# Performance work log

Measured on AMD Instinct MI355X. Metric: run time of the kernel, lower is better.

Reference implementation:

```python
import jax, jax.numpy as jnp
import numpy as np

NUM_EMBEDDINGS = 8192
EMBEDDING_DIM = 256
COMMITMENT_COST = 0.25


def setup_inputs() -> dict:
    key = jax.random.key(0)
    k1, k2 = jax.random.split(key)
    inputs = jax.random.normal(k1, (32, 32, 32, EMBEDDING_DIM), dtype=jnp.float32)
    # flax nn.initializers.uniform(scale=1/num_embeddings) -> U[0, scale)
    embeddings = jax.random.uniform(
        k2, (NUM_EMBEDDINGS, EMBEDDING_DIM), dtype=jnp.float32,
        minval=0.0, maxval=1.0 / NUM_EMBEDDINGS)
    return {"inputs": inputs, "embeddings": embeddings}


def reference(inputs, embeddings):
    flat_input = inputs.reshape(-1, EMBEDDING_DIM)  # [N, D]
    distances = (jnp.sum(flat_input ** 2, axis=1, keepdims=True)
                 - 2.0 * jnp.dot(flat_input, embeddings.T)
                 + jnp.sum(embeddings ** 2, axis=1)[None, :])
    encoding_indices = jnp.argmin(distances, axis=1)  # [N]
    quantized = embeddings[encoding_indices]  # [N, D]

    e_latent_loss = jnp.mean((jax.lax.stop_gradient(quantized) - flat_input) ** 2)
    q_latent_loss = jnp.mean((quantized - jax.lax.stop_gradient(flat_input)) ** 2)
    vq_loss = q_latent_loss + COMMITMENT_COST * e_latent_loss

    # straight-through estimator
    quantized_st = flat_input + jax.lax.stop_gradient(quantized - flat_input)
    quantized_st = quantized_st.reshape(inputs.shape)

    # perplexity via codebook usage histogram (avoids materializing one-hot)
    counts = jnp.zeros((NUM_EMBEDDINGS,), dtype=flat_input.dtype).at[encoding_indices].add(1.0)
    avg_probs = counts / flat_input.shape[0]
    perplexity = jnp.exp(-jnp.sum(avg_probs * jnp.log(avg_probs + 1e-10)))

    return quantized_st, vq_loss, perplexity, encoding_indices
```

## Files before the change

### kernel.cpp

```cpp
#include <hip/hip_runtime.h>
#include <math.h>

#pragma clang fp contract(off)

#define N_ROWS 32768
#define DIM    256
#define K_EMB  8192
#define BCAP   2048
#define NSUB   256

typedef float  f32x4  __attribute__((ext_vector_type(4)));
typedef short  bf16x8 __attribute__((ext_vector_type(8)));

__device__ __forceinline__ void gl_lds16(const uint4* g, uint4* l) {
  __builtin_amdgcn_global_load_lds(
      (const __attribute__((address_space(1))) unsigned int*)g,
      (__attribute__((address_space(3))) unsigned int*)l,
      16, 0, 0);
}

__device__ __forceinline__ unsigned bf_rne(float f) {
  unsigned u = __float_as_uint(f);
  return (u + 0x7fffu + ((u >> 16) & 1u)) >> 16;
}
__device__ __forceinline__ unsigned pack2(float lo, float hi) {
  return bf_rne(lo) | (bf_rne(hi) << 16);
}

__device__ __forceinline__ float np_pw128_sumsq(const float* __restrict__ a) {
  float4 v0 = *(const float4*)(a);
  float4 v1 = *(const float4*)(a + 4);
  float r0 = v0.x*v0.x, r1 = v0.y*v0.y, r2 = v0.z*v0.z, r3 = v0.w*v0.w;
  float r4 = v1.x*v1.x, r5 = v1.y*v1.y, r6 = v1.z*v1.z, r7 = v1.w*v1.w;
  for (int i = 8; i < 128; i += 8) {
    float4 w0 = *(const float4*)(a + i);
    float4 w1 = *(const float4*)(a + i + 4);
    r0 += w0.x*w0.x; r1 += w0.y*w0.y; r2 += w0.z*w0.z; r3 += w0.w*w0.w;
    r4 += w1.x*w1.x; r5 += w1.y*w1.y; r6 += w1.z*w1.z; r7 += w1.w*w1.w;
  }
  return ((r0+r1)+(r2+r3))+((r4+r5)+(r6+r7));
}

__global__ __launch_bounds__(256) void vq_sumsq(const float* __restrict__ src,
                                                float* __restrict__ dst, int nrows) {
  int gid  = blockIdx.x * 256 + threadIdx.x;
  int row  = gid >> 1, half = gid & 1;
  if (row >= nrows) return;
  float s = np_pw128_sumsq(src + (size_t)row * DIM + half * 128);
  float o = __shfl_xor(s, 1);
  if (half == 0) dst[row] = s + o;
}

__global__ __launch_bounds__(256) void vq_prep(
    const float* __restrict__ X, const float* __restrict__ E,
    float* __restrict__ A, float* __restrict__ C, uint4* __restrict__ Eb,
    unsigned* __restrict__ hist, unsigned* __restrict__ bcnt,
    unsigned* __restrict__ ovf, unsigned long long* __restrict__ best) {
  const int b = blockIdx.x;
  if (b < 1024) {
    int t = b * 256 + threadIdx.x;
    int tile = t >> 6, l = t & 63;
    int cfg = tile >> 3, ks = tile & 7;
    int code = cfg * 16 + (l & 15);
    int k0 = (ks * 4 + (l >> 4)) * 8;
    const float4* src = (const float4*)(E + (size_t)code * DIM + k0);
    float4 a = src[0], bb = src[1];
    uint4 o;
    o.x = pack2(a.x, a.y);  o.y = pack2(a.z, a.w);
    o.z = pack2(bb.x, bb.y); o.w = pack2(bb.z, bb.w);
    Eb[t] = o;
  } else if (b < 1280) {
    int gid = (b - 1024) * 256 + threadIdx.x;
    int row = gid >> 1, half = gid & 1;
    float s = np_pw128_sumsq(X + (size_t)row * DIM + half * 128);
    float o = __shfl_xor(s, 1);
    if (half == 0) A[row] = s + o;
  } else if (b < 1344) {
    int gid = (b - 1280) * 256 + threadIdx.x;
    int row = gid >> 1, half = gid & 1;
    float s = np_pw128_sumsq(E + (size_t)row * DIM + half * 128);
    float o = __shfl_xor(s, 1);
    if (half == 0) C[row] = s + o;
  } else {
    int i = (b - 1344) * 256 + threadIdx.x;
    ovf[i]  = 0u;
    best[i] = ~0ull;
    if (i < K_EMB) hist[i] = 0u;
    if (i < NSUB)  bcnt[i] = 0u;
  }
}

__global__ __launch_bounds__(256)
__attribute__((amdgpu_waves_per_eu(2, 2)))
void vq_mfma_slice(
    const float* __restrict__ X, const uint4* __restrict__ Eb,
    unsigned short* __restrict__ submax_t) {
  __shared__ __align__(16) unsigned short es[2][64 * 256];

  const int tid   = threadIdx.x;
  const int lane  = tid & 63, w = tid >> 6;
  const int lr    = lane & 15, lg = lane >> 4;
  const int wcg   = w & 1;
  const int wxg   = w >> 1;
  const int rb    = blockIdx.x >> 1;
  const int slice = blockIdx.x & 1;
  const int row0  = rb * 128;

  const uint4* ebase = Eb + (size_t)slice * 131072;

#pragma unroll
  for (int i = 0; i < 8; ++i) {
    int u = tid + i * 256;
    gl_lds16(ebase + u, ((uint4*)&es[0][0]) + u);
  }

  bf16x8 bx[4][8];
#pragma unroll
  for (int rf = 0; rf < 4; ++rf) {
    const float* xr = X + (size_t)(row0 + wxg * 64 + rf * 16 + lr) * DIM;
#pragma unroll
    for (int ks = 0; ks < 8; ++ks) {
      int k0 = (ks * 4 + lg) * 8;
      float4 a = *(const float4*)(xr + k0);
      float4 b = *(const float4*)(xr + k0 + 4);
      uint4 o;
      o.x = pack2(a.x, a.y); o.y = pack2(a.z, a.w);
      o.z = pack2(b.x, b.y); o.w = pack2(b.z, b.w);
      bx[rf][ks] = *(bf16x8*)&o;
    }
  }
  __syncthreads();

  for (int c = 0; c < 64; ++c) {
    const int cur = c & 1;
    if (c + 1 < 64) {
#pragma unroll
      for (int i = 0; i < 8; ++i) {
        int u = tid + i * 256;
        gl_lds16(ebase + (size_t)(c + 1) * 2048 + u, ((uint4*)&es[cur ^ 1][0]) + u);
      }
    }

    f32x4 acc[2][4];
#pragma unroll
    for (int ce = 0; ce < 2; ++ce)
#pragma unroll
      for (int rf = 0; rf < 4; ++rf)
        acc[ce][rf] = (f32x4){0.f, 0.f, 0.f, 0.f};

    const unsigned short* eb = &es[cur][0];
#pragma unroll
    for (int ks = 0; ks < 8; ++ks) {
      bf16x8 ev0 = *(const bf16x8*)(eb + (((wcg * 2 + 0) * 8 + ks) * 64 + lane) * 8);
      bf16x8 ev1 = *(const bf16x8*)(eb + (((wcg * 2 + 1) * 8 + ks) * 64 + lane) * 8);
#pragma unroll
      for (int rf = 0; rf < 4; ++rf) {
        acc[0][rf] = __builtin_amdgcn_mfma_f32_16x16x32_bf16(ev0, bx[rf][ks], acc[0][rf], 0, 0, 0);
        acc[1][rf] = __builtin_amdgcn_mfma_f32_16x16x32_bf16(ev1, bx[rf][ks], acc[1][rf], 0, 0, 0);
      }
    }

    const int sub = slice * 128 + c * 2 + wcg;
#pragma unroll
    for (int rf = 0; rf < 4; ++rf) {
      float m = acc[0][rf][0];
#pragma unroll
      for (int ce = 0; ce < 2; ++ce)
#pragma unroll
        for (int rg = 0; rg < 4; ++rg)
          if (ce | rg) m = fmaxf(m, acc[ce][rf][rg]);
      m = fmaxf(m, __shfl_xor(m, 16));
      m = fmaxf(m, __shfl_xor(m, 32));
      if (lg == 0) {
        int qi = (int)((m + 0.0625f) * 524288.0f);
        qi = qi < 0 ? 0 : (qi > 65535 ? 65535 : qi);
        submax_t[(size_t)sub * N_ROWS + row0 + wxg * 64 + rf * 16 + lr] =
            (unsigned short)qi;
      }
    }

    asm volatile("s_waitcnt vmcnt(4)" ::: "memory");
    __builtin_amdgcn_s_barrier();
  }
}

__global__ __launch_bounds__(256) void vq_flag(
    const unsigned short* __restrict__ submax_t, const float* __restrict__ A,
    unsigned* __restrict__ bcnt, unsigned short* __restrict__ buckets,
    unsigned* __restrict__ ovf) {
  __shared__ unsigned cntA[NSUB], baseS[NSUB], cntC[NSUB];
  const int t   = threadIdx.x;
  const int row = blockIdx.x * 256 + t;
  cntA[t] = 0u; cntC[t] = 0u;
  __syncthreads();

  int mq = 0;
  for (int s = 0; s < NSUB; ++s) {
    int q = submax_t[(size_t)s * N_ROWS + row];
    mq = q > mq ? q : mq;
  }
  const int wq   = (int)((sqrtf(A[row]) * 4e-6f + 9.6e-5f) * 524288.0f) + 2;
  const int thrq = mq - wq;

  for (int s = 0; s < NSUB; ++s)
    if ((int)submax_t[(size_t)s * N_ROWS + row] >= thrq) atomicAdd(&cntA[s], 1u);
  __syncthreads();

  baseS[t] = atomicAdd(&bcnt[t], cntA[t]);
  __syncthreads();

  for (int s = 0; s < NSUB; ++s) {
    if ((int)submax_t[(size_t)s * N_ROWS + row] >= thrq) {
      unsigned p = baseS[s] + atomicAdd(&cntC[s], 1u);
      if (p < BCAP) buckets[s * BCAP + p] = (unsigned short)row;
      else          ovf[row] = 1u;
    }
  }
}

__global__ __launch_bounds__(256) void vq_exact(
    const float* __restrict__ X, const float* __restrict__ E,
    const float* __restrict__ A, const float* __restrict__ C,
    const unsigned* __restrict__ bcnt, const unsigned short* __restrict__ buckets,
    unsigned long long* __restrict__ best) {
  __shared__ float e_lds[32][260];
  __shared__ float xr[4][4][256];
  const int tid  = threadIdx.x;
  const int lane = tid & 63, w = tid >> 6;
  const int bk   = blockIdx.x >> 2, q4 = blockIdx.x & 3;

#pragma unroll
  for (int i = 0; i < 8; ++i) {
    int u = tid + i * 256;
    int code = u >> 6, koff = (u & 63) * 4;
    float4 v = *(const float4*)(E + (size_t)(bk * 32 + code) * DIM + koff);
    *(float4*)(&e_lds[code][koff]) = v;
  }
  __syncthreads();

  int n = (int)bcnt[bk]; if (n > BCAP) n = BCAP;
  const int   half = lane >> 5, c32 = lane & 31;
  const int   j  = bk * 32 + c32;
  const float cj = C[j];

  for (int p0 = q4 * 16 + w * 4; p0 < n; p0 += 64) {
    int valid[4], rows[4];
#pragma unroll
    for (int k = 0; k < 4; ++k) {
      int pk = p0 + k;
      valid[k] = (pk < n);
      rows[k]  = buckets[(size_t)bk * BCAP + (pk < n ? pk : p0)];
    }
#pragma unroll
    for (int k = 0; k < 4; ++k)
      *(float4*)(&xr[w][k][lane * 4]) =
          *(const float4*)(X + (size_t)rows[k] * DIM + lane * 4);
    asm volatile("s_waitcnt lgkmcnt(0)" ::: "memory");

    float acc0 = 0.f, acc1 = 0.f;
    const float* xa = &xr[w][half][0];
    const float* xb = &xr[w][half + 2][0];
#pragma unroll 4
    for (int kq = 0; kq < 64; ++kq) {
      float4 ev = *(const float4*)(&e_lds[c32][kq * 4]);
      float4 x0 = *(const float4*)(xa + kq * 4);
      float4 x1 = *(const float4*)(xb + kq * 4);
      acc0 = fmaf(x0.x, ev.x, acc0); acc0 = fmaf(x0.y, ev.y, acc0);
      acc0 = fmaf(x0.z, ev.z, acc0); acc0 = fmaf(x0.w, ev.w, acc0);
      acc1 = fmaf(x1.x, ev.x, acc1); acc1 = fmaf(x1.y, ev.y, acc1);
      acc1 = fmaf(x1.z, ev.z, acc1); acc1 = fmaf(x1.w, ev.w, acc1);
    }
    float d0 = (A[rows[half]]     - 2.0f * acc0) + cj;
    float d1 = (A[rows[half + 2]] - 2.0f * acc1) + cj;
    int   j0 = j, j1 = j;
#pragma unroll
    for (int mm = 1; mm < 32; mm <<= 1) {
      float od = __shfl_xor(d0, mm); int oj = __shfl_xor(j0, mm);
      if (od < d0 || (od == d0 && oj < j0)) { d0 = od; j0 = oj; }
      od = __shfl_xor(d1, mm); oj = __shfl_xor(j1, mm);
      if (od < d1 || (od == d1 && oj < j1)) { d1 = od; j1 = oj; }
    }
    if (c32 == 0) {
      if (valid[half])
        atomicMin(&best[rows[half]],
                  ((unsigned long long)__float_as_uint(d0) << 32) | (unsigned)j0);
      if (valid[half + 2])
        atomicMin(&best[rows[half + 2]],
                  ((unsigned long long)__float_as_uint(d1) << 32) | (unsigned)j1);
    }
  }
}

__global__ __launch_bounds__(256) void vq_finish(
    const float* __restrict__ X, const float* __restrict__ E,
    const float* __restrict__ A, const float* __restrict__ C,
    const unsigned* __restrict__ ovf, const unsigned long long* __restrict__ best,
    int* __restrict__ idx_out, float* __restrict__ idxf_out) {
  int row  = blockIdx.x * 256 + threadIdx.x;
  int lane = threadIdx.x & 63;
  unsigned o = ovf[row];
  if (!o) {
    int j = (int)(best[row] & 0xffffffffu);
    idx_out[row]  = j;
    idxf_out[row] = (float)j;
  }
  unsigned long long m = __ballot(o != 0u);
  while (m) {
    int src  = __ffsll((long long)m) - 1;
    int orow = __shfl(row, src);
    const float a_r = A[orow];
    const float4* X4 = (const float4*)(X + (size_t)orow * DIM);
    float bd = INFINITY; int bj = 0x7fffffff;
    for (int jj = lane; jj < K_EMB; jj += 64) {
      const float4* E4 = (const float4*)(E + (size_t)jj * DIM);
      float acc = 0.f;
      for (int kb = 0; kb < 64; ++kb) {
        float4 xv = X4[kb], ev = E4[kb];
        acc = fmaf(xv.x, ev.x, acc); acc = fmaf(xv.y, ev.y, acc);
        acc = fmaf(xv.z, ev.z, acc); acc = fmaf(xv.w, ev.w, acc);
      }
      float d = (a_r - 2.0f * acc) + C[jj];
      if (d < bd || (d == bd && jj < bj)) { bd = d; bj = jj; }
    }
    for (int mm = 1; mm < 64; mm <<= 1) {
      float od = __shfl_xor(bd, mm);
      int   oj = __shfl_xor(bj, mm);
      if (od < bd || (od == bd && oj < bj)) { bd = od; bj = oj; }
    }
    if (lane == 0) { idx_out[orow] = bj; idxf_out[orow] = (float)bj; }
    m &= m - 1;
  }
}

__global__ __launch_bounds__(256) void vq_argmin(const float* __restrict__ X,
                                                 const float* __restrict__ E,
                                                 const float* __restrict__ A,
                                                 const float* __restrict__ C,
                                                 int* __restrict__ idx_out,
                                                 float* __restrict__ idxf_out) {
  __shared__ float4 xs4[64 * 64];
  const int tid  = threadIdx.x;
  const int rl   = tid >> 2;
  const int cg   = tid & 3;
  const int row0 = blockIdx.x * 64;

  const float4* Xg = (const float4*)(X + (size_t)row0 * DIM);
  for (int it = 0; it < 16; ++it) {
    int f4 = tid + it * 256;
    float4 v = Xg[f4];
    int r = f4 >> 6, kb = f4 & 63;
    xs4[r * 64 + (kb ^ (r & 7))] = v;
  }
  __syncthreads();

  const float a_r = A[row0 + rl];
  const int   swq = rl & 7;
  const float4* xrow = xs4 + rl * 64;

  float bd = INFINITY;
  int   bj = 0x7fffffff;

  for (int tile = 0; tile < K_EMB; tile += 16) {
    const int j0 = tile + cg * 4;
    const float4* e0 = (const float4*)(E + (size_t)(j0 + 0) * DIM);
    const float4* e1 = (const float4*)(E + (size_t)(j0 + 1) * DIM);
    const float4* e2 = (const float4*)(E + (size_t)(j0 + 2) * DIM);
    const float4* e3 = (const float4*)(E + (size_t)(j0 + 3) * DIM);
    float acc0 = 0.f, acc1 = 0.f, acc2 = 0.f, acc3 = 0.f;
#pragma unroll 4
    for (int kb = 0; kb < 64; ++kb) {
      const float4 xv = xrow[kb ^ swq];
      const float4 q0 = e0[kb], q1 = e1[kb], q2 = e2[kb], q3 = e3[kb];
      acc0 = fmaf(xv.x, q0.x, acc0); acc0 = fmaf(xv.y, q0.y, acc0);
      acc0 = fmaf(xv.z, q0.z, acc0); acc0 = fmaf(xv.w, q0.w, acc0);
      acc1 = fmaf(xv.x, q1.x, acc1); acc1 = fmaf(xv.y, q1.y, acc1);
      acc1 = fmaf(xv.z, q1.z, acc1); acc1 = fmaf(xv.w, q1.w, acc1);
      acc2 = fmaf(xv.x, q2.x, acc2); acc2 = fmaf(xv.y, q2.y, acc2);
      acc2 = fmaf(xv.z, q2.z, acc2); acc2 = fmaf(xv.w, q2.w, acc2);
      acc3 = fmaf(xv.x, q3.x, acc3); acc3 = fmaf(xv.y, q3.y, acc3);
      acc3 = fmaf(xv.z, q3.z, acc3); acc3 = fmaf(xv.w, q3.w, acc3);
    }
    const float d0 = (a_r - 2.0f * acc0) + C[j0 + 0];
    const float d1 = (a_r - 2.0f * acc1) + C[j0 + 1];
    const float d2 = (a_r - 2.0f * acc2) + C[j0 + 2];
    const float d3 = (a_r - 2.0f * acc3) + C[j0 + 3];
    if (d0 < bd) { bd = d0; bj = j0 + 0; }
    if (d1 < bd) { bd = d1; bj = j0 + 1; }
    if (d2 < bd) { bd = d2; bj = j0 + 2; }
    if (d3 < bd) { bd = d3; bj = j0 + 3; }
  }
  for (int m = 1; m < 4; m <<= 1) {
    float od = __shfl_xor(bd, m);
    int   oj = __shfl_xor(bj, m);
    if (od < bd || (od == bd && oj < bj)) { bd = od; bj = oj; }
  }
  if (cg == 0) {
    int row = row0 + rl;
    idx_out[row]  = bj;
    idxf_out[row] = (float)bj;
  }
}

__global__ __launch_bounds__(256) void vq_quant(const float* __restrict__ X,
                                                const float* __restrict__ E,
                                                const int* __restrict__ idx,
                                                float* __restrict__ out_qst,
                                                double* __restrict__ partials,
                                                unsigned* __restrict__ hist) {
  int gid  = blockIdx.x * 256 + threadIdx.x;
  int base = gid * 4;
  int row  = base >> 8;
  int k    = base & 255;
  int j    = idx[row];
  if (k == 0) atomicAdd(&hist[j], 1u);
  const float4 xv = *(const float4*)(X + (size_t)base);
  const float4 ev = *(const float4*)(E + (size_t)j * DIM + k);
  float4 o;
  float d0 = ev.x - xv.x, d1 = ev.y - xv.y, d2 = ev.z - xv.z, d3 = ev.w - xv.w;
  o.x = xv.x + d0; o.y = xv.y + d1; o.z = xv.z + d2; o.w = xv.w + d3;
  double s = (double)d0 * d0 + (double)d1 * d1 + (double)d2 * d2 + (double)d3 * d3;
  *(float4*)(out_qst + (size_t)base) = o;

  for (int m = 32; m; m >>= 1) s += __shfl_xor(s, m);
  __shared__ double wsum[4];
  int lane = threadIdx.x & 63, w = threadIdx.x >> 6;
  if (lane == 0) wsum[w] = s;
  __syncthreads();
  if (threadIdx.x == 0)
    partials[blockIdx.x] = (wsum[0] + wsum[1]) + (wsum[2] + wsum[3]);
}

__global__ void vq_zero(unsigned* counts) {
  int i = blockIdx.x * 256 + threadIdx.x;
  if (i < K_EMB) counts[i] = 0u;
}

__global__ __launch_bounds__(256) void vq_scalars(const double* __restrict__ partials,
                                                  const unsigned* __restrict__ counts,
                                                  float* __restrict__ out_loss,
                                                  float* __restrict__ out_perp) {
  __shared__ double red[256];
  int t = threadIdx.x;
  double s = 0.0;
  for (int i = t; i < 8192; i += 256) s += partials[i];
  red[t] = s;
  __syncthreads();
  for (int o = 128; o; o >>= 1) { if (t < o) red[t] += red[t + o]; __syncthreads(); }
  double mse = red[0] / (double)((size_t)N_ROWS * DIM);
  __syncthreads();

  double p = 0.0;
  for (int i = t; i < K_EMB; i += 256) {
    double pr = (double)counts[i] / (double)N_ROWS;
    p += pr * log(pr + 1e-10);
  }
  red[t] = p;
  __syncthreads();
  for (int o = 128; o; o >>= 1) { if (t < o) red[t] += red[t + o]; __syncthreads(); }
  if (t == 0) {
    float m = (float)mse;
    out_loss[0] = m + 0.25f * m;
    out_perp[0] = (float)exp(-red[0]);
  }
}

extern "C" void kernel_launch(void* const* d_in, const int* in_sizes, int n_in,
                              void* d_out, int out_size, void* d_ws, size_t ws_size,
                              hipStream_t stream) {
  const float* X = (const float*)d_in[0];
  const float* E = (const float*)d_in[1];
  float* out  = (float*)d_out;
  float* qst  = out;
  float* loss = out + 8388608;
  float* perp = out + 8388609;
  float* idxf = out + 8388610;

  float*    A        = (float*)d_ws;
  float*    C        = (float*)((char*)d_ws + 131072);
  int*      idx      = (int*)((char*)d_ws + 163840);
  unsigned* hist     = (unsigned*)((char*)d_ws + 294912);
  double*   partials = (double*)((char*)d_ws + 327680);

  if (ws_size >= 22807552) {
    unsigned long long* best = (unsigned long long*)((char*)d_ws + 393216);
    unsigned* ovf          = (unsigned*)((char*)d_ws + 655360);
    unsigned* bcnt         = (unsigned*)((char*)d_ws + 786432);
    unsigned short* bucket = (unsigned short*)((char*)d_ws + 787456);
    uint4*    Eb           = (uint4*)((char*)d_ws + 1836032);
    unsigned short* sm     = (unsigned short*)((char*)d_ws + 6030336);

    vq_prep       <<<1472, 256, 0, stream>>>(X, E, A, C, Eb, hist, bcnt, ovf, best);
    vq_mfma_slice <<<512,  256, 0, stream>>>(X, Eb, sm);
    vq_flag       <<<128,  256, 0, stream>>>(sm, A, bcnt, bucket, ovf);
    vq_exact      <<<1024, 256, 0, stream>>>(X, E, A, C, bcnt, bucket, best);
    vq_finish     <<<128,  256, 0, stream>>>(X, E, A, C, ovf, best, idx, idxf);
  } else {
    vq_zero   <<<32,  256, 0, stream>>>(hist);
    vq_sumsq  <<<256, 256, 0, stream>>>(X, A, N_ROWS);
    vq_sumsq  <<<64,  256, 0, stream>>>(E, C, K_EMB);
    vq_argmin <<<512, 256, 0, stream>>>(X, E, A, C, idx, idxf);
  }

  vq_quant  <<<8192, 256, 0, stream>>>(X, E, idx, qst, partials, hist);
  vq_scalars<<<1,    256, 0, stream>>>(partials, hist, loss, perp);
}
```

Before: 345.2 us.

## Fuse candidate flagging into MFMA slice kernel via last-block completion counter

Removes the separate vq_flag launch. Each row block's two slice CTAs bump a per-row-block counter, and the second one to finish scans the submax values for its 128 rows and writes the candidate buckets. The candidate window constant is also narrowed, which should shrink the bucket lists and the exact-rescoring work in vq_exact. The risks are a serialized tail in the MFMA kernel with only half the threads doing the flag work, and a tighter window that may miss true argmins.

```diff
diff --git a/kernel.cpp b/kernel.cpp
--- a/kernel.cpp
+++ b/kernel.cpp
@@ -25,6 +25,10 @@
 }
 __device__ __forceinline__ unsigned pack2(float lo, float hi) {
   return bf_rne(lo) | (bf_rne(hi) << 16);
+}
+
+__device__ __forceinline__ int window_q(float a) {
+  return (int)((sqrtf(a) * 4e-6f + 5.0e-5f) * 524288.0f) + 2;
 }
 
 __device__ __forceinline__ float np_pw128_sumsq(const float* __restrict__ a) {
@@ -55,7 +59,8 @@
     const float* __restrict__ X, const float* __restrict__ E,
     float* __restrict__ A, float* __restrict__ C, uint4* __restrict__ Eb,
     unsigned* __restrict__ hist, unsigned* __restrict__ bcnt,
-    unsigned* __restrict__ ovf, unsigned long long* __restrict__ best) {
+    unsigned* __restrict__ ovf, unsigned long long* __restrict__ best,
+    unsigned* __restrict__ done) {
   const int b = blockIdx.x;
   if (b < 1024) {
     int t = b * 256 + threadIdx.x;
@@ -87,6 +92,7 @@
     best[i] = ~0ull;
     if (i < K_EMB) hist[i] = 0u;
     if (i < NSUB)  bcnt[i] = 0u;
+    if (i < 256)   done[i] = 0u;
   }
 }
 
@@ -94,8 +100,12 @@
 __attribute__((amdgpu_waves_per_eu(2, 2)))
 void vq_mfma_slice(
     const float* __restrict__ X, const uint4* __restrict__ Eb,
-    unsigned short* __restrict__ submax_t) {
+    const float* __restrict__ A, unsigned short* __restrict__ submax_t,
+    unsigned* __restrict__ done, unsigned* __restrict__ bcnt,
+    unsigned short* __restrict__ buckets, unsigned* __restrict__ ovf) {
   __shared__ __align__(16) unsigned short es[2][64 * 256];
+  __shared__ unsigned cntA[NSUB], baseS[NSUB], cntC[NSUB];
+  __shared__ unsigned sdone;
 
   const int tid   = threadIdx.x;
   const int lane  = tid & 63, w = tid >> 6;
@@ -182,38 +192,43 @@
     asm volatile("s_waitcnt vmcnt(4)" ::: "memory");
     __builtin_amdgcn_s_barrier();
   }
-}
-
-__global__ __launch_bounds__(256) void vq_flag(
-    const unsigned short* __restrict__ submax_t, const float* __restrict__ A,
-    unsigned* __restrict__ bcnt, unsigned short* __restrict__ buckets,
-    unsigned* __restrict__ ovf) {
-  __shared__ unsigned cntA[NSUB], baseS[NSUB], cntC[NSUB];
-  const int t   = threadIdx.x;
-  const int row = blockIdx.x * 256 + t;
-  cntA[t] = 0u; cntC[t] = 0u;
-  __syncthreads();
-
-  int mq = 0;
-  for (int s = 0; s < NSUB; ++s) {
-    int q = submax_t[(size_t)s * N_ROWS + row];
-    mq = q > mq ? q : mq;
-  }
-  const int wq   = (int)((sqrtf(A[row]) * 4e-6f + 9.6e-5f) * 524288.0f) + 2;
-  const int thrq = mq - wq;
-
-  for (int s = 0; s < NSUB; ++s)
-    if ((int)submax_t[(size_t)s * N_ROWS + row] >= thrq) atomicAdd(&cntA[s], 1u);
-  __syncthreads();
-
-  baseS[t] = atomicAdd(&bcnt[t], cntA[t]);
-  __syncthreads();
-
-  for (int s = 0; s < NSUB; ++s) {
-    if ((int)submax_t[(size_t)s * N_ROWS + row] >= thrq) {
-      unsigned p = baseS[s] + atomicAdd(&cntC[s], 1u);
-      if (p < BCAP) buckets[s * BCAP + p] = (unsigned short)row;
-      else          ovf[row] = 1u;
+
+  asm volatile("s_waitcnt vmcnt(0)" ::: "memory");
+  __threadfence();
+  __syncthreads();
+  if (tid == 0) sdone = atomicAdd(&done[rb], 1u);
+  __syncthreads();
+  if (sdone == 0) return;
+  __threadfence();
+
+  cntA[tid] = 0u; cntC[tid] = 0u;
+  __syncthreads();
+
+  int thrq = 0;
+  if (tid < 128) {
+    const int row = row0 + tid;
+    const unsigned short* sr = submax_t + row;
+    int mq = 0;
+    for (int s = 0; s < NSUB; ++s) {
+      int q = sr[(size_t)s * N_ROWS];
+      mq = q > mq ? q : mq;
+    }
+    thrq = mq - window_q(A[row]);
+    for (int s = 0; s < NSUB; ++s)
+      if ((int)sr[(size_t)s * N_ROWS] >= thrq) atomicAdd(&cntA[s], 1u);
+  }
+  __syncthreads();
+  baseS[tid] = atomicAdd(&bcnt[tid], cntA[tid]);
+  __syncthreads();
+  if (tid < 128) {
+    const int row = row0 + tid;
+    const unsigned short* sr = submax_t + row;
+    for (int s = 0; s < NSUB; ++s) {
+      if ((int)sr[(size_t)s * N_ROWS] >= thrq) {
+        unsigned p = baseS[s] + atomicAdd(&cntC[s], 1u);
+        if (p < BCAP) buckets[s * BCAP + p] = (unsigned short)row;
+        else          ovf[row] = 1u;
+      }
     }
   }
 }
@@ -481,17 +496,17 @@
   unsigned* hist     = (unsigned*)((char*)d_ws + 294912);
   double*   partials = (double*)((char*)d_ws + 327680);
 
-  if (ws_size >= 22807552) {
+  if (ws_size >= 22808576) {
     unsigned long long* best = (unsigned long long*)((char*)d_ws + 393216);
     unsigned* ovf          = (unsigned*)((char*)d_ws + 655360);
     unsigned* bcnt         = (unsigned*)((char*)d_ws + 786432);
     unsigned short* bucket = (unsigned short*)((char*)d_ws + 787456);
     uint4*    Eb           = (uint4*)((char*)d_ws + 1836032);
     unsigned short* sm     = (unsigned short*)((char*)d_ws + 6030336);
-
-    vq_prep       <<<1472, 256, 0, stream>>>(X, E, A, C, Eb, hist, bcnt, ovf, best);
-    vq_mfma_slice <<<512,  256, 0, stream>>>(X, Eb, sm);
-    vq_flag       <<<128,  256, 0, stream>>>(sm, A, bcnt, bucket, ovf);
+    unsigned* done         = (unsigned*)((char*)d_ws + 22807552);
+
+    vq_prep       <<<1472, 256, 0, stream>>>(X, E, A, C, Eb, hist, bcnt, ovf, best, done);
+    vq_mfma_slice <<<512,  256, 0, stream>>>(X, Eb, A, sm, done, bcnt, bucket, ovf);
     vq_exact      <<<1024, 256, 0, stream>>>(X, E, A, C, bcnt, bucket, best);
     vq_finish     <<<128,  256, 0, stream>>>(X, E, A, C, ovf, best, idx, idxf);
   } else {
```

Measured after the change: 395.2 us. 14.5% more time.
